# Kernel tuning notes

Measured on AMD Instinct MI355X. Metric: run time of the kernel, lower is better.

The kernel has to match this reference:

```python
import jax, jax.numpy as jnp
from jax import lax
import numpy as np

H = 64   # hidden_dim
R = 32   # rank


def setup_inputs() -> dict:
    key = jax.random.key(0)
    ks = jax.random.split(key, 18)
    B, C, T = 64, 256, 512
    s = 0.1
    f32 = jnp.float32
    return {
        "x": jax.random.normal(ks[0], (B, C, T), f32),
        "y": jax.random.normal(ks[1], (B, C, 1), f32),
        # GRU layer 0 (input_size=1)
        "W_ih0": (jax.random.normal(ks[2], (3 * H, 1), f32) * s),
        "W_hh0": (jax.random.normal(ks[3], (3 * H, H), f32) * s),
        "b_ih0": (jax.random.normal(ks[4], (3 * H,), f32) * s),
        "b_hh0": (jax.random.normal(ks[5], (3 * H,), f32) * s),
        # GRU layer 1 (input_size=H)
        "W_ih1": (jax.random.normal(ks[6], (3 * H, H), f32) * s),
        "W_hh1": (jax.random.normal(ks[7], (3 * H, H), f32) * s),
        "b_ih1": (jax.random.normal(ks[8], (3 * H,), f32) * s),
        "b_hh1": (jax.random.normal(ks[9], (3 * H,), f32) * s),
        # heads
        "W_mean": (jax.random.normal(ks[10], (1, H), f32) * s),
        "b_mean": (jax.random.normal(ks[11], (1,), f32) * s),
        "W_d": (jax.random.normal(ks[12], (1, H), f32) * s),
        "b_d": (jax.random.normal(ks[13], (1,), f32) * s),
        "W_v": (jax.random.normal(ks[14], (R, H), f32) * s),
        "b_v": (jax.random.normal(ks[15], (R,), f32) * s),
    }


def _gru_cell(xin, h, Wih, Whh, bih, bhh):
    # PyTorch GRU cell. xin: [N, in], h: [N, H]
    gx = xin @ Wih.T + bih            # [N, 3H]
    gh = h @ Whh.T + bhh              # [N, 3H]
    r = jax.nn.sigmoid(gx[:, :H] + gh[:, :H])
    z = jax.nn.sigmoid(gx[:, H:2 * H] + gh[:, H:2 * H])
    n = jnp.tanh(gx[:, 2 * H:] + r * gh[:, 2 * H:])
    return (1.0 - z) * n + z * h


def reference(x, y, W_ih0, W_hh0, b_ih0, b_hh0, W_ih1, W_hh1, b_ih1, b_hh1,
              W_mean, b_mean, W_d, b_d, W_v, b_v):
    B, C, T = x.shape
    N = B * C
    # Original loops the GRU over channels; channels are independent sequences,
    # so batch them all: [T, N, 1]
    xs = x.reshape(N, T).T[:, :, None]

    def step(carry, xt):
        h0, h1 = carry
        h0 = _gru_cell(xt, h0, W_ih0, W_hh0, b_ih0, b_hh0)
        h1 = _gru_cell(h0, h1, W_ih1, W_hh1, b_ih1, b_hh1)
        return (h0, h1), None

    h0 = jnp.zeros((N, H), x.dtype)
    (_, hT), _ = lax.scan(step, (h0, h0), xs)   # hT: last output of top layer
    hT = hT.reshape(B, C, H)

    mu = hT @ W_mean.T + b_mean                 # [B, C, 1]
    v = hT @ W_v.T + b_v                        # [B, C, R]
    d = jnp.log1p(jnp.exp(hT @ W_d.T + b_d))[..., 0]   # softplus, [B, C]

    sigma = jnp.einsum('bcr,bkr->bck', v, v) + jnp.eye(C, dtype=x.dtype) * d[:, :, None]
    resid = y - mu                              # [B, C, 1]
    inv = jnp.linalg.inv(sigma)
    quad = jnp.einsum('bci,bck,bkj->b', resid, inv, resid)
    logdet = jnp.linalg.slogdet(sigma)[1]
    return jnp.mean(quad + logdet)
```

## Files before the change

### kernel.cpp

```cpp
#include <hip/hip_runtime.h>

typedef __attribute__((ext_vector_type(8))) _Float16 f16x8;
typedef __attribute__((ext_vector_type(4))) float f32x4;

namespace {

constexpr int H_ = 64;
constexpr int R_ = 32;
constexpr int B_ = 64;
constexpr int C_ = 256;
constexpr int T_ = 512;
constexpr int N_ = B_ * C_;

constexpr float NLOG2E  = -1.44269504088896f;
constexpr float N2LOG2E = -2.88539008177793f;

#define MFMA16(a, b, c) __builtin_amdgcn_mfma_f32_16x16x32_f16((a), (b), (c), 0, 0, 0)

__device__ __forceinline__ float gru_combine(float h, float t_n, float t_z) {
    float vn  = 1.0f + t_n;
    float num = __fmaf_rn(h, vn, (1.0f - t_n) * t_z);
    float den = vn * (1.0f + t_z);
    return num * __builtin_amdgcn_rcpf(den);
}

__global__ void pack_weights_kernel(const float* __restrict__ Whh0,
                                    const float* __restrict__ Wih1,
                                    const float* __restrict__ Whh1,
                                    _Float16* __restrict__ packed)
{
    const int b = blockIdx.x;
    const int w = b / 18, f = b % 18;
    const int l = threadIdx.x;
    const int c = l & 15, g = l >> 4;
    const int hb = w * 16;
    const int kk = f & 1;
    const float* src = Whh0;
    int row = 0;
    float scale = 1.0f;
    switch (f >> 1) {
        case 0: src = Whh0; row = hb + c;        break;
        case 1: src = Whh0; row = 64 + hb + c;   break;
        case 2: src = Whh0; row = 128 + hb + c;  scale = N2LOG2E; break;
        case 3: src = Wih1; row = hb + c;        break;
        case 4: src = Whh1; row = hb + c;        break;
        case 5: src = Wih1; row = 64 + hb + c;   break;
        case 6: src = Whh1; row = 64 + hb + c;   break;
        case 7: src = Wih1; row = 128 + hb + c;  scale = N2LOG2E; break;
        case 8: src = Whh1; row = 128 + hb + c;  scale = N2LOG2E; break;
    }
    _Float16* dst = packed + ((size_t)(w * 18 + f) * 512) + (size_t)l * 8;
    #pragma unroll
    for (int j = 0; j < 8; ++j) {
        int k = kk * 32 + g * 8 + j;
        dst[j] = (_Float16)(src[row * 64 + k] * scale);
    }
}


#define PHASE_L0(PP, XB, DT)                                                  \
  do {                                                                        \
    const _Float16* h0rd = &h0s[(PP) ^ 1][0][0];                              \
    f16x8 a00 = *(const f16x8*)(h0rd + c * 72 + g * 8);                       \
    f16x8 a01 = *(const f16x8*)(h0rd + c * 72 + 32 + g * 8);                  \
    __builtin_amdgcn_s_setprio(1);                                            \
    f32x4 accr = MFMA16(a01, Br[1], MFMA16(a00, Br[0], zv));                  \
    f32x4 accz = MFMA16(a01, Br[3], MFMA16(a00, Br[2], zv));                  \
    f32x4 accn = MFMA16(a01, Br[5], MFMA16(a00, Br[4], vb0nh));               \
    __builtin_amdgcn_s_setprio(0);                                            \
    float4 xq = *(const float4*)(&xs_[XB][DT][g * 4]);                        \
    _Pragma("unroll")                                                         \
    for (int q = 0; q < 4; ++q) {                                             \
      int seq = g * 4 + q;                                                    \
      float xv = ((const float*)&xq)[q];                                      \
      float tr = __builtin_amdgcn_exp2f(                                      \
          __fmaf_rn(__fmaf_rn(xv, wr0, accr[q]), NLOG2E, cb0r));              \
      float r  = __builtin_amdgcn_rcpf(1.0f + tr);                            \
      float tz = __builtin_amdgcn_exp2f(                                      \
          __fmaf_rn(__fmaf_rn(xv, wz0, accz[q]), NLOG2E, cb0z));              \
      float tn = __builtin_amdgcn_exp2f(                                      \
          __fmaf_rn(r, accn[q], __fmaf_rn(xv, wn0, b0nx)));                   \
      float hn = gru_combine(h0st[q], tn, tz);                                \
      h0st[q] = hn;                                                           \
      h0s[PP][seq][hid] = (_Float16)hn;                                       \
    }                                                                         \
  } while (0)

#define PHASE_L1(PP, DOSTORE)                                                 \
  do {                                                                        \
    const _Float16* h0rd = &h0s[(PP) ^ 1][0][0];                              \
    const _Float16* h1rd = &h1s[(PP) ^ 1][0][0];                              \
    f16x8 a00 = *(const f16x8*)(h0rd + c * 72 + g * 8);                       \
    f16x8 a01 = *(const f16x8*)(h0rd + c * 72 + 32 + g * 8);                  \
    f16x8 ah0 = *(const f16x8*)(h1rd + c * 72 + g * 8);                       \
    f16x8 ah1 = *(const f16x8*)(h1rd + c * 72 + 32 + g * 8);                  \
    __builtin_amdgcn_s_setprio(1);                                            \
    f32x4 r1  = MFMA16(ah1, Br[3], MFMA16(ah0, Br[2],                         \
                MFMA16(a01, Br[1], MFMA16(a00, Br[0], zv))));                 \
    f32x4 z1  = MFMA16(ah1, Br[7], MFMA16(ah0, Br[6],                         \
                MFMA16(a01, Br[5], MFMA16(a00, Br[4], zv))));                 \
    f32x4 xn1 = MFMA16(a01, Br[9],  MFMA16(a00, Br[8],  vb1nx));              \
    f32x4 hn1 = MFMA16(ah1, Br[11], MFMA16(ah0, Br[10], vb1nh));              \
    __builtin_amdgcn_s_setprio(0);                                            \
    _Pragma("unroll")                                                         \
    for (int q = 0; q < 4; ++q) {                                             \
      int seq = g * 4 + q;                                                    \
      float tr = __builtin_amdgcn_exp2f(__fmaf_rn(r1[q], NLOG2E, cb1r));      \
      float r  = __builtin_amdgcn_rcpf(1.0f + tr);                            \
      float tz = __builtin_amdgcn_exp2f(__fmaf_rn(z1[q], NLOG2E, cb1z));      \
      float tn = __builtin_amdgcn_exp2f(__fmaf_rn(r, hn1[q], xn1[q]));        \
      float hn = gru_combine(h1st[q], tn, tz);                                \
      h1st[q] = hn;                                                           \
      if (DOSTORE) h1s[PP][seq][hid] = (_Float16)hn;                          \
    }                                                                         \
  } while (0)

__global__ __launch_bounds__(512, 4)
void gru_mfma_kernel(const float* __restrict__ x,
                     const _Float16* __restrict__ packedW,
                     const float* __restrict__ Wih0,
                     const float* __restrict__ bih0,
                     const float* __restrict__ bhh0,
                     const float* __restrict__ bih1,
                     const float* __restrict__ bhh1,
                     float* __restrict__ hT_out)
{
    __shared__ __align__(16) _Float16 h0s[2][16][72];
    __shared__ __align__(16) _Float16 h1s[2][16][72];
    __shared__ __align__(16) float xs_[2][32][20];

    const int tid = threadIdx.x;
    const int l = tid & 63;
    const int w = tid >> 6;
    const bool isL0 = (w < 4);
    const int sl = isL0 ? w : (w - 4);
    const int c = l & 15, g = (l >> 4) & 3;
    const int hid = sl * 16 + c;
    const int n0 = blockIdx.x * 16;

    f16x8 Br[12];
    {
        const f16x8* bp = (const f16x8*)(packedW + (size_t)sl * 18 * 512);
        if (isL0) {
            #pragma unroll
            for (int f = 0; f < 6; ++f) Br[f] = bp[f * 64 + l];
        } else {
            #pragma unroll
            for (int f = 0; f < 12; ++f) Br[f] = bp[(6 + f) * 64 + l];
        }
    }

    float wr0 = 0.f, wz0 = 0.f, wn0 = 0.f, cb0r = 0.f, cb0z = 0.f;
    float b0nh = 0.f, b0nx = 0.f, cb1r = 0.f, cb1z = 0.f, b1nx = 0.f, b1nh = 0.f;
    if (isL0) {
        wr0 = Wih0[hid]; wz0 = Wih0[64 + hid];
        wn0 = N2LOG2E * Wih0[128 + hid];
        cb0r = NLOG2E * (bhh0[hid] + bih0[hid]);
        cb0z = NLOG2E * (bhh0[64 + hid] + bih0[64 + hid]);
        b0nh = N2LOG2E * bhh0[128 + hid];
        b0nx = N2LOG2E * bih0[128 + hid];
    } else {
        cb1r = NLOG2E * (bih1[hid] + bhh1[hid]);
        cb1z = NLOG2E * (bih1[64 + hid] + bhh1[64 + hid]);
        b1nx = N2LOG2E * bih1[128 + hid];
        b1nh = N2LOG2E * bhh1[128 + hid];
    }
    const f32x4 vb0nh = {b0nh, b0nh, b0nh, b0nh};
    const f32x4 vb1nx = {b1nx, b1nx, b1nx, b1nx};
    const f32x4 vb1nh = {b1nh, b1nh, b1nh, b1nh};

    for (int p = tid; p < 2 * 16 * 72; p += 512) {
        (&h0s[0][0][0])[p] = (_Float16)0.0f;
        (&h1s[0][0][0])[p] = (_Float16)0.0f;
    }
    float h0st[4] = {0.f, 0.f, 0.f, 0.f};
    float h1st[4] = {0.f, 0.f, 0.f, 0.f};

    auto stage_x = [&](int t0) {
        int buf = (t0 >> 5) & 1;
        int tb = tid & 31;
        int ss = tid >> 5;
        xs_[buf][tb][ss] = x[(size_t)(n0 + ss) * T_ + t0 + tb];
    };

    const f32x4 zv = {0.f, 0.f, 0.f, 0.f};

    stage_x(0);
    __syncthreads();
    if (isL0) PHASE_L0(0, 0, 0);

    for (int p = 1; p < T_ - 1; p += 2) {
        __syncthreads();
        if (isL0) PHASE_L0(1, (p >> 5) & 1, p & 31); else PHASE_L1(1, true);
        if ((p & 31) == 31) stage_x(p + 1);
        __syncthreads();
        if (isL0) PHASE_L0(0, ((p + 1) >> 5) & 1, (p + 1) & 31);
        else      PHASE_L1(0, true);
    }

    __syncthreads();
    if (isL0) PHASE_L0(1, 1, 31); else PHASE_L1(1, true);

    __syncthreads();
    if (!isL0) {
        PHASE_L1(0, false);
        #pragma unroll
        for (int q = 0; q < 4; ++q) {
            int seq = g * 4 + q;
            hT_out[(size_t)(n0 + seq) * H_ + hid] = h1st[q];
        }
    }
}

__global__ __launch_bounds__(256)
void heads_kernel(const float* __restrict__ hT,
                  const float* __restrict__ y,
                  const float* __restrict__ Wm, const float* __restrict__ bm,
                  const float* __restrict__ Wd, const float* __restrict__ bd,
                  const float* __restrict__ Wv, const float* __restrict__ bv,
                  float* __restrict__ v_out,
                  float* __restrict__ dd_out,
                  float* __restrict__ r_out)
{
    const int n = blockIdx.x * 256 + threadIdx.x;
    const float* h = hT + (size_t)n * H_;

    float hreg[H_];
    #pragma unroll
    for (int j = 0; j < H_; j += 4) {
        float4 q = *(const float4*)(h + j);
        hreg[j] = q.x; hreg[j + 1] = q.y; hreg[j + 2] = q.z; hreg[j + 3] = q.w;
    }
    float mu = bm[0], dv = bd[0];
    #pragma unroll
    for (int j = 0; j < H_; ++j) {
        mu = __fmaf_rn(Wm[j], hreg[j], mu);
        dv = __fmaf_rn(Wd[j], hreg[j], dv);
    }
    r_out[n]  = y[n] - mu;
    dd_out[n] = log1pf(__expf(dv));

    for (int k = 0; k < R_; ++k) {
        float acc = bv[k];
        #pragma unroll
        for (int j = 0; j < H_; ++j)
            acc = __fmaf_rn(Wv[k * H_ + j], hreg[j], acc);
        v_out[(size_t)n * R_ + k] = acc;
    }
}

__device__ __forceinline__ float block_reduce_sum256(float* red, int tid, float val)
{
    red[tid] = val;
    __syncthreads();
    for (int off = 128; off > 0; off >>= 1) {
        if (tid < off) red[tid] += red[tid + off];
        __syncthreads();
    }
    float r = red[0];
    __syncthreads();
    return r;
}

__global__ __launch_bounds__(256)
void woodbury_kernel(const float* __restrict__ v_in,
                     const float* __restrict__ dd_in,
                     const float* __restrict__ r_in,
                     float* __restrict__ batch_out)
{
    __shared__ float Vl[C_][R_ + 1];
    __shared__ float Vw[C_][R_ + 1];
    __shared__ float wi[C_];
    __shared__ float rl[C_];
    __shared__ float red[256];
    __shared__ float MA[R_][R_ + 1];
    __shared__ float uA[R_], yA[R_], wA[R_];

    const int tid = threadIdx.x;
    const int nb  = blockIdx.x * C_;

    for (int p = tid; p < C_ * R_; p += 256) {
        int cc = p >> 5, k = p & 31;
        Vl[cc][k] = v_in[(size_t)(nb + cc) * R_ + k];
    }
    float dval = dd_in[nb + tid];
    float winv = 1.0f / dval;
    float rv   = r_in[nb + tid];
    wi[tid] = winv;
    rl[tid] = rv;
    __syncthreads();

    for (int p = tid; p < C_ * R_; p += 256) {
        int cc = p >> 5, k = p & 31;
        Vw[cc][k] = Vl[cc][k] * wi[cc];
    }
    __syncthreads();

    float slogd = block_reduce_sum256(red, tid, __logf(dval));
    float rDr   = block_reduce_sum256(red, tid, rv * rv * winv);

    #pragma unroll
    for (int e = 0; e < 4; ++e) {
        int p = tid + e * 256;
        int i = p >> 5, j = p & 31;
        float acc = (i == j) ? 1.0f : 0.0f;
        for (int cc = 0; cc < C_; ++cc)
            acc = __fmaf_rn(Vw[cc][i], Vl[cc][j], acc);
        MA[i][j] = acc;
    }
    if (tid < R_) {
        float acc = 0.0f;
        for (int cc = 0; cc < C_; ++cc)
            acc = __fmaf_rn(Vw[cc][tid], rl[cc], acc);
        uA[tid] = acc;
    }
    __syncthreads();

    for (int k = 0; k < R_; ++k) {
        if (tid == 0) MA[k][k] = sqrtf(MA[k][k]);
        __syncthreads();
        if (tid > k && tid < R_) MA[tid][k] /= MA[k][k];
        __syncthreads();
        if (tid > k && tid < R_) {
            float ljk = MA[tid][k];
            for (int i2 = k + 1; i2 <= tid; ++i2)
                MA[tid][i2] -= ljk * MA[i2][k];
        }
        __syncthreads();
    }
    float ldm = block_reduce_sum256(red, tid,
                    (tid < R_) ? 2.0f * __logf(MA[tid][tid]) : 0.0f);

    if (tid == 0) {
        for (int k = 0; k < R_; ++k) {
            float sv = uA[k];
            for (int i2 = 0; i2 < k; ++i2) sv -= MA[k][i2] * yA[i2];
            yA[k] = sv / MA[k][k];
        }
        for (int k = R_ - 1; k >= 0; --k) {
            float sv = yA[k];
            for (int i2 = k + 1; i2 < R_; ++i2) sv -= MA[i2][k] * wA[i2];
            wA[k] = sv / MA[k][k];
        }
        float uw = 0.0f;
        for (int k = 0; k < R_; ++k) uw += wA[k] * uA[k];
        batch_out[blockIdx.x] = (rDr - uw) + slogd + ldm;
    }
}

__global__ void finalize_kernel(const float* __restrict__ bws, float* __restrict__ out)
{
    float v = bws[threadIdx.x];
    #pragma unroll
    for (int off = 32; off > 0; off >>= 1)
        v += __shfl_down(v, off, 64);
    if (threadIdx.x == 0) out[0] = v * (1.0f / 64.0f);
}

}

extern "C" void kernel_launch(void* const* d_in, const int* in_sizes, int n_in,
                              void* d_out, int out_size, void* d_ws, size_t ws_size,
                              hipStream_t stream)
{
    const float* x    = (const float*)d_in[0];
    const float* y    = (const float*)d_in[1];
    const float* Wih0 = (const float*)d_in[2];
    const float* Whh0 = (const float*)d_in[3];
    const float* bih0 = (const float*)d_in[4];
    const float* bhh0 = (const float*)d_in[5];
    const float* Wih1 = (const float*)d_in[6];
    const float* Whh1 = (const float*)d_in[7];
    const float* bih1 = (const float*)d_in[8];
    const float* bhh1 = (const float*)d_in[9];
    const float* Wm   = (const float*)d_in[10];
    const float* bm   = (const float*)d_in[11];
    const float* Wd   = (const float*)d_in[12];
    const float* bd   = (const float*)d_in[13];
    const float* Wv   = (const float*)d_in[14];
    const float* bv   = (const float*)d_in[15];

    char* ws = (char*)d_ws;
    float*    hT     = (float*)(ws + 0);
    float*    v_ws   = (float*)(ws + 4194304);
    float*    dd_ws  = (float*)(ws + 6291456);
    float*    r_ws   = (float*)(ws + 6356992);
    float*    b_ws   = (float*)(ws + 6422528);
    _Float16* packed = (_Float16*)(ws + 6423552);

    pack_weights_kernel<<<72, 64, 0, stream>>>(Whh0, Wih1, Whh1, packed);
    gru_mfma_kernel<<<N_ / 16, 512, 0, stream>>>(
        x, packed, Wih0, bih0, bhh0, bih1, bhh1, hT);
    heads_kernel<<<N_ / 256, 256, 0, stream>>>(
        hT, y, Wm, bm, Wd, bd, Wv, bv, v_ws, dd_ws, r_ws);
    woodbury_kernel<<<B_, 256, 0, stream>>>(v_ws, dd_ws, r_ws, b_ws);
    finalize_kernel<<<1, 64, 0, stream>>>(b_ws, (float*)d_out);
}
```

Before: 949.2 us.

## Transpose MFMA operands so each lane owns four hidden units and vectorize stores

New measurement: 1.030 ms. +8.5%, slower.

```diff
diff --git a/kernel.cpp b/kernel.cpp
--- a/kernel.cpp
+++ b/kernel.cpp
@@ -1,6 +1,7 @@
 #include <hip/hip_runtime.h>
 
 typedef __attribute__((ext_vector_type(8))) _Float16 f16x8;
+typedef __attribute__((ext_vector_type(4))) _Float16 f16x4;
 typedef __attribute__((ext_vector_type(4))) float f32x4;
 
 namespace {
@@ -18,9 +19,9 @@
 #define MFMA16(a, b, c) __builtin_amdgcn_mfma_f32_16x16x32_f16((a), (b), (c), 0, 0, 0)
 
 __device__ __forceinline__ float gru_combine(float h, float t_n, float t_z) {
-    float vn  = 1.0f + t_n;
-    float num = __fmaf_rn(h, vn, (1.0f - t_n) * t_z);
-    float den = vn * (1.0f + t_z);
+    float tz1 = 1.0f + t_z;
+    float num = __fmaf_rn(t_n, h - t_z, h + t_z);
+    float den = __fmaf_rn(t_n, tz1, tz1);
     return num * __builtin_amdgcn_rcpf(den);
 }
 
@@ -37,7 +38,7 @@
     const int kk = f & 1;
     const float* src = Whh0;
     int row = 0;
-    float scale = 1.0f;
+    float scale = NLOG2E;
     switch (f >> 1) {
         case 0: src = Whh0; row = hb + c;        break;
         case 1: src = Whh0; row = 64 + hb + c;   break;
@@ -64,26 +65,24 @@
     f16x8 a00 = *(const f16x8*)(h0rd + c * 72 + g * 8);                       \
     f16x8 a01 = *(const f16x8*)(h0rd + c * 72 + 32 + g * 8);                  \
     __builtin_amdgcn_s_setprio(1);                                            \
-    f32x4 accr = MFMA16(a01, Br[1], MFMA16(a00, Br[0], zv));                  \
-    f32x4 accz = MFMA16(a01, Br[3], MFMA16(a00, Br[2], zv));                  \
-    f32x4 accn = MFMA16(a01, Br[5], MFMA16(a00, Br[4], vb0nh));               \
+    f32x4 accr = MFMA16(Br[1], a01, MFMA16(Br[0], a00, vcb0r));               \
+    f32x4 accz = MFMA16(Br[3], a01, MFMA16(Br[2], a00, vcb0z));               \
+    f32x4 accn = MFMA16(Br[5], a01, MFMA16(Br[4], a00, vb0nh));               \
     __builtin_amdgcn_s_setprio(0);                                            \
-    float4 xq = *(const float4*)(&xs_[XB][DT][g * 4]);                        \
+    float xv = xs_[XB][DT][c];                                                \
+    f16x4 hv;                                                                 \
     _Pragma("unroll")                                                         \
     for (int q = 0; q < 4; ++q) {                                             \
-      int seq = g * 4 + q;                                                    \
-      float xv = ((const float*)&xq)[q];                                      \
-      float tr = __builtin_amdgcn_exp2f(                                      \
-          __fmaf_rn(__fmaf_rn(xv, wr0, accr[q]), NLOG2E, cb0r));              \
+      float tr = __builtin_amdgcn_exp2f(__fmaf_rn(xv, wr0n[q], accr[q]));     \
       float r  = __builtin_amdgcn_rcpf(1.0f + tr);                            \
-      float tz = __builtin_amdgcn_exp2f(                                      \
-          __fmaf_rn(__fmaf_rn(xv, wz0, accz[q]), NLOG2E, cb0z));              \
+      float tz = __builtin_amdgcn_exp2f(__fmaf_rn(xv, wz0n[q], accz[q]));     \
       float tn = __builtin_amdgcn_exp2f(                                      \
-          __fmaf_rn(r, accn[q], __fmaf_rn(xv, wn0, b0nx)));                   \
+          __fmaf_rn(r, accn[q], __fmaf_rn(xv, wn0s[q], b0nxs[q])));           \
       float hn = gru_combine(h0st[q], tn, tz);                                \
       h0st[q] = hn;                                                           \
-      h0s[PP][seq][hid] = (_Float16)hn;                                       \
+      hv[q] = (_Float16)hn;                                                   \
     }                                                                         \
+    *(f16x4*)&h0s[PP][c][hb4] = hv;                                           \
   } while (0)
 
 #define PHASE_L1(PP, DOSTORE)                                                 \
@@ -95,24 +94,25 @@
     f16x8 ah0 = *(const f16x8*)(h1rd + c * 72 + g * 8);                       \
     f16x8 ah1 = *(const f16x8*)(h1rd + c * 72 + 32 + g * 8);                  \
     __builtin_amdgcn_s_setprio(1);                                            \
-    f32x4 r1  = MFMA16(ah1, Br[3], MFMA16(ah0, Br[2],                         \
-                MFMA16(a01, Br[1], MFMA16(a00, Br[0], zv))));                 \
-    f32x4 z1  = MFMA16(ah1, Br[7], MFMA16(ah0, Br[6],                         \
-                MFMA16(a01, Br[5], MFMA16(a00, Br[4], zv))));                 \
-    f32x4 xn1 = MFMA16(a01, Br[9],  MFMA16(a00, Br[8],  vb1nx));              \
-    f32x4 hn1 = MFMA16(ah1, Br[11], MFMA16(ah0, Br[10], vb1nh));              \
+    f32x4 r1  = MFMA16(Br[3], ah1, MFMA16(Br[2], ah0,                         \
+                MFMA16(Br[1], a01, MFMA16(Br[0], a00, vcb1r))));              \
+    f32x4 z1  = MFMA16(Br[7], ah1, MFMA16(Br[6], ah0,                         \
+                MFMA16(Br[5], a01, MFMA16(Br[4], a00, vcb1z))));              \
+    f32x4 xn1 = MFMA16(Br[9],  a01, MFMA16(Br[8],  a00, vb1nx));              \
+    f32x4 hn1 = MFMA16(Br[11], ah1, MFMA16(Br[10], ah0, vb1nh));              \
     __builtin_amdgcn_s_setprio(0);                                            \
+    f16x4 hv;                                                                 \
     _Pragma("unroll")                                                         \
     for (int q = 0; q < 4; ++q) {                                             \
-      int seq = g * 4 + q;                                                    \
-      float tr = __builtin_amdgcn_exp2f(__fmaf_rn(r1[q], NLOG2E, cb1r));      \
+      float tr = __builtin_amdgcn_exp2f(r1[q]);                               \
       float r  = __builtin_amdgcn_rcpf(1.0f + tr);                            \
-      float tz = __builtin_amdgcn_exp2f(__fmaf_rn(z1[q], NLOG2E, cb1z));      \
+      float tz = __builtin_amdgcn_exp2f(z1[q]);                               \
       float tn = __builtin_amdgcn_exp2f(__fmaf_rn(r, hn1[q], xn1[q]));        \
       float hn = gru_combine(h1st[q], tn, tz);                                \
       h1st[q] = hn;                                                           \
-      if (DOSTORE) h1s[PP][seq][hid] = (_Float16)hn;                          \
+      hv[q] = (_Float16)hn;                                                   \
     }                                                                         \
+    if (DOSTORE) *(f16x4*)&h1s[PP][c][hb4] = hv;                              \
   } while (0)
 
 __global__ __launch_bounds__(512, 4)
@@ -133,9 +133,10 @@
     const int l = tid & 63;
     const int w = tid >> 6;
     const bool isL0 = (w < 4);
-    const int sl = isL0 ? w : (w - 4);
+    const int sl = w & 3;
     const int c = l & 15, g = (l >> 4) & 3;
-    const int hid = sl * 16 + c;
+    const int hb = sl * 16;
+    const int hb4 = hb + g * 4;
     const int n0 = blockIdx.x * 16;
 
     f16x8 Br[12];
@@ -150,24 +151,27 @@
         }
     }
 
-    float wr0 = 0.f, wz0 = 0.f, wn0 = 0.f, cb0r = 0.f, cb0z = 0.f;
-    float b0nh = 0.f, b0nx = 0.f, cb1r = 0.f, cb1z = 0.f, b1nx = 0.f, b1nh = 0.f;
-    if (isL0) {
-        wr0 = Wih0[hid]; wz0 = Wih0[64 + hid];
-        wn0 = N2LOG2E * Wih0[128 + hid];
-        cb0r = NLOG2E * (bhh0[hid] + bih0[hid]);
-        cb0z = NLOG2E * (bhh0[64 + hid] + bih0[64 + hid]);
-        b0nh = N2LOG2E * bhh0[128 + hid];
-        b0nx = N2LOG2E * bih0[128 + hid];
-    } else {
-        cb1r = NLOG2E * (bih1[hid] + bhh1[hid]);
-        cb1z = NLOG2E * (bih1[64 + hid] + bhh1[64 + hid]);
-        b1nx = N2LOG2E * bih1[128 + hid];
-        b1nh = N2LOG2E * bhh1[128 + hid];
-    }
-    const f32x4 vb0nh = {b0nh, b0nh, b0nh, b0nh};
-    const f32x4 vb1nx = {b1nx, b1nx, b1nx, b1nx};
-    const f32x4 vb1nh = {b1nh, b1nh, b1nh, b1nh};
+    f32x4 wr0n = {0,0,0,0}, wz0n = {0,0,0,0}, wn0s = {0,0,0,0}, b0nxs = {0,0,0,0};
+    f32x4 vcb0r = {0,0,0,0}, vcb0z = {0,0,0,0}, vb0nh = {0,0,0,0};
+    f32x4 vcb1r = {0,0,0,0}, vcb1z = {0,0,0,0}, vb1nx = {0,0,0,0}, vb1nh = {0,0,0,0};
+    #pragma unroll
+    for (int q = 0; q < 4; ++q) {
+        int hq = hb4 + q;
+        if (isL0) {
+            wr0n[q]  = NLOG2E  * Wih0[hq];
+            wz0n[q]  = NLOG2E  * Wih0[64 + hq];
+            wn0s[q]  = N2LOG2E * Wih0[128 + hq];
+            b0nxs[q] = N2LOG2E * bih0[128 + hq];
+            vcb0r[q] = NLOG2E  * (bhh0[hq] + bih0[hq]);
+            vcb0z[q] = NLOG2E  * (bhh0[64 + hq] + bih0[64 + hq]);
+            vb0nh[q] = N2LOG2E * bhh0[128 + hq];
+        } else {
+            vcb1r[q] = NLOG2E  * (bih1[hq] + bhh1[hq]);
+            vcb1z[q] = NLOG2E  * (bih1[64 + hq] + bhh1[64 + hq]);
+            vb1nx[q] = N2LOG2E * bih1[128 + hq];
+            vb1nh[q] = N2LOG2E * bhh1[128 + hq];
+        }
+    }
 
     for (int p = tid; p < 2 * 16 * 72; p += 512) {
         (&h0s[0][0][0])[p] = (_Float16)0.0f;
@@ -183,8 +187,6 @@
         xs_[buf][tb][ss] = x[(size_t)(n0 + ss) * T_ + t0 + tb];
     };
 
-    const f32x4 zv = {0.f, 0.f, 0.f, 0.f};
-
     stage_x(0);
     __syncthreads();
     if (isL0) PHASE_L0(0, 0, 0);
@@ -204,11 +206,9 @@
     __syncthreads();
     if (!isL0) {
         PHASE_L1(0, false);
-        #pragma unroll
-        for (int q = 0; q < 4; ++q) {
-            int seq = g * 4 + q;
-            hT_out[(size_t)(n0 + seq) * H_ + hid] = h1st[q];
-        }
+        float4 o;
+        o.x = h1st[0]; o.y = h1st[1]; o.z = h1st[2]; o.w = h1st[3];
+        *(float4*)&hT_out[(size_t)(n0 + c) * H_ + hb4] = o;
     }
 }
 
```
